# Kernel optimization log

Hardware: AMD Instinct MI355X
Metric: run time of the kernel (lower is better)

Reference implementation:

```python
import jax, jax.numpy as jnp
import numpy as np

# Fixed tetrahedral (kanchor=4) rotation->anchor permutation table, taken verbatim
# from the docstring in the original source (trace_idx_ori).
TRACE_IDX_ORI = jnp.array([
    [0, 1, 2, 3], [0, 2, 3, 1], [0, 3, 1, 2],
    [1, 2, 0, 3], [1, 0, 3, 2], [1, 3, 2, 0],
    [2, 3, 0, 1], [2, 0, 1, 3], [2, 1, 3, 0],
    [3, 1, 0, 2], [3, 0, 2, 1], [3, 2, 1, 0]], dtype=jnp.int32)

B, A, N, M, D, H = 1, 4, 384, 384, 256, 8
C = D // H  # d_model_per_head = 32
NR = TRACE_IDX_ORI.shape[0]  # 12 rotations


def _project_heads(x, W, b):
    # x: (b, a, n, d) -> (b, a, h, n, c)
    y = x @ W.T + b
    bb, aa, nn, _ = y.shape
    return y.reshape(bb, aa, nn, H, C).transpose(0, 1, 3, 2, 4)


def setup_inputs() -> dict:
    key = jax.random.key(0)
    ks = jax.random.split(key, 6)
    s = 1.0 / np.sqrt(D).astype(np.float32)
    return {
        "input_q": jax.random.normal(ks[0], (B, A, N, D), dtype=jnp.float32),
        "input_k": jax.random.normal(ks[1], (B, A, M, D), dtype=jnp.float32),
        "input_v": jax.random.normal(ks[2], (B, A, M, D), dtype=jnp.float32),
        "Wq": jax.random.normal(ks[3], (D, D), dtype=jnp.float32) * s,
        "bq": jnp.zeros((D,), dtype=jnp.float32),
        "Wk": jax.random.normal(ks[4], (D, D), dtype=jnp.float32) * s,
        "bk": jnp.zeros((D,), dtype=jnp.float32),
        "Wv": jax.random.normal(ks[5], (D, D), dtype=jnp.float32) * s,
        "bv": jnp.zeros((D,), dtype=jnp.float32),
    }


def reference(input_q, input_k, input_v, Wq, bq, Wk, bk, Wv, bv):
    # Step 0: linear projections + split heads.  q,k,v: (b, a, h, n|m, c)
    q = _project_heads(input_q, Wq, bq)
    k = _project_heads(input_k, Wk, bk)
    v = _project_heads(input_v, Wv, bv)

    # Step 1: per-anchor-pair local attention scores: (b, a, e, h, n, m)
    scores_ae = jnp.einsum('bahnc,behmc->baehnm', q, k) / jnp.sqrt(
        jnp.asarray(C, dtype=q.dtype))

    # Step 2: rotation-wise gather (attn_mode='r_soft', alternative_impl=False).
    # For rotation r, query anchor a attends to key anchor trace_idx_ori[r, a]:
    # scores_rot[b, r, a] = scores_ae[b, a, trace_idx_ori[r, a]]  -> (b, nr, a, h, n, m)
    a_idx = jnp.arange(A, dtype=jnp.int32)[None, :]  # (1, A) broadcasts vs (NR, A)
    scores_rot = scores_ae[:, a_idx, TRACE_IDX_ORI]

    # Global rotation attention: pool over anchors/heads/points (attn_r_summ='mean',
    # attn_r_multihead=False), make non-negative ('sq'), normalize over rotations.
    pooled = jnp.mean(scores_rot, axis=(2, 3, 4, 5))  # (b, nr)
    pos = pooled * pooled
    attn_r = pos / jnp.sum(pos, axis=-1, keepdims=True)  # (b, nr)

    # Step 3+4: softmax over key points per rotation, gather values per rotation,
    # then weight by the global rotation attention.
    attn_local = jax.nn.softmax(scores_rot, axis=-1)  # (b, nr, a, h, n, m)
    v_rot = v[:, TRACE_IDX_ORI]  # (b, nr, a, h, m, c)
    hidden = jnp.einsum('br,brahnm,brahmc->bahnc', attn_r, attn_local, v_rot)

    # Merge heads: (b, a, h, n, c) -> (b, a, n, h*c)
    out = hidden.transpose(0, 1, 3, 2, 4).reshape(B, A, N, D)
    return out
```

## Files before the change

kernel.cpp:

```cpp
#include <hip/hip_runtime.h>
#include <hip/hip_bf16.h>

typedef __attribute__((ext_vector_type(8))) short s8x8;
typedef __attribute__((ext_vector_type(4))) float f32x4;

__device__ __forceinline__ ushort f2bf(float x) {
    union { float f; unsigned u; } c; c.f = x;
    unsigned r = c.u + 0x7FFFu + ((c.u >> 16) & 1u);
    return (ushort)(r >> 16);
}
__device__ __forceinline__ float bf2f(ushort b) {
    union { unsigned u; float f; } c; c.u = ((unsigned)b) << 16;
    return c.f;
}

__global__ __launch_bounds__(128) void proj_mfma_kernel(
    const float* __restrict__ Xq, const float* __restrict__ Xk,
    const float* __restrict__ Xv,
    const float* __restrict__ Wq, const float* __restrict__ bq,
    const float* __restrict__ Wk, const float* __restrict__ bk,
    const float* __restrict__ Wv, const float* __restrict__ bv,
    ushort* __restrict__ qh, ushort* __restrict__ ql,
    ushort* __restrict__ kh, ushort* __restrict__ kl,
    ushort* __restrict__ vh)
{
    __shared__ ushort smem[2][16384];

    const int z = blockIdx.z;
    const float* X    = (z == 0) ? Xq : (z == 1) ? Xk : Xv;
    const float* W    = (z == 0) ? Wq : (z == 1) ? Wk : Wv;
    const float* bias = (z == 0) ? bq : (z == 1) ? bk : bv;

    const int tid  = threadIdx.x;
    const int row0 = blockIdx.x * 64;
    const int col0 = blockIdx.y * 64;

    #pragma unroll
    for (int i = 0; i < 32; ++i) {
        const int idx4 = tid + 128 * i;
        const int col  = idx4 >> 6;
        const int k4   = (idx4 & 63) * 4;
        const float4 wv = *(const float4*)&W[(col0 + col) * 256 + k4];
        const int kk = k4 >> 5;
        const int lg = (k4 >> 3) & 3;
        const int i0 = k4 & 7;
        const int base = ((kk * 4 + lg) * 64 + col) * 8 + i0;
        ushort hb[4], lb[4];
        const float w0[4] = {wv.x, wv.y, wv.z, wv.w};
        #pragma unroll
        for (int j = 0; j < 4; ++j) {
            hb[j] = f2bf(w0[j]);
            lb[j] = f2bf(w0[j] - bf2f(hb[j]));
        }
        *(uint2*)&smem[0][base] = *(const uint2*)&hb[0];
        *(uint2*)&smem[1][base] = *(const uint2*)&lb[0];
    }
    __syncthreads();

    const int wave = tid >> 6;
    const int lane = tid & 63;
    const int lg   = lane >> 4;
    const int ll   = lane & 15;

    f32x4 acc[2][4];
    #pragma unroll
    for (int r = 0; r < 2; ++r)
        #pragma unroll
        for (int c = 0; c < 4; ++c) acc[r][c] = (f32x4){0.f, 0.f, 0.f, 0.f};

    for (int kk = 0; kk < 8; ++kk) {
        s8x8 ah[2], al[2];
        #pragma unroll
        for (int rt = 0; rt < 2; ++rt) {
            const int row = row0 + wave * 32 + rt * 16 + ll;
            const float* xp = &X[(size_t)row * 256 + kk * 32 + lg * 8];
            const float4 x0 = *(const float4*)&xp[0];
            const float4 x1 = *(const float4*)&xp[4];
            const float xv[8] = {x0.x, x0.y, x0.z, x0.w, x1.x, x1.y, x1.z, x1.w};
            #pragma unroll
            for (int j = 0; j < 8; ++j) {
                const ushort hb = f2bf(xv[j]);
                ah[rt][j] = (short)hb;
                al[rt][j] = (short)f2bf(xv[j] - bf2f(hb));
            }
        }
        #pragma unroll
        for (int ct = 0; ct < 4; ++ct) {
            const int boff = ((kk * 4 + lg) * 64 + ct * 16 + ll) * 8;
            const s8x8 bh = *(const s8x8*)&smem[0][boff];
            const s8x8 bl = *(const s8x8*)&smem[1][boff];
            #pragma unroll
            for (int rt = 0; rt < 2; ++rt) {
                acc[rt][ct] = __builtin_amdgcn_mfma_f32_16x16x32_bf16(ah[rt], bh, acc[rt][ct], 0, 0, 0);
                acc[rt][ct] = __builtin_amdgcn_mfma_f32_16x16x32_bf16(al[rt], bh, acc[rt][ct], 0, 0, 0);
                acc[rt][ct] = __builtin_amdgcn_mfma_f32_16x16x32_bf16(ah[rt], bl, acc[rt][ct], 0, 0, 0);
            }
        }
    }

    float bct[4];
    #pragma unroll
    for (int ct = 0; ct < 4; ++ct) bct[ct] = bias[col0 + ct * 16 + ll];

    if (z != 2) {
        #pragma unroll
        for (int rt = 0; rt < 2; ++rt) {
            #pragma unroll
            for (int j = 0; j < 4; ++j) {
                const int row = row0 + wave * 32 + rt * 16 + lg * 4 + j;
                const int ae = row / 384;
                const int n = row - ae * 384;
                #pragma unroll
                for (int ct = 0; ct < 4; ++ct) {
                    const int d = col0 + ct * 16 + ll;
                    const int hd = d >> 5;
                    const int c = d & 31;
                    const float v = acc[rt][ct][j] + bct[ct];
                    const ushort hb = f2bf(v);
                    const ushort lb = f2bf(v - bf2f(hb));
                    if (z == 0) {
                        const size_t idx = ((size_t)((ae * 8 + hd) * 384 + n)) * 32 + c;
                        qh[idx] = hb; ql[idx] = lb;
                    } else {
                        const size_t idx =
                            ((size_t)(((ae * 8 + hd) * 4 + (c >> 3)) * 384 + n)) * 8 + (c & 7);
                        kh[idx] = hb; kl[idx] = lb;
                    }
                }
            }
        }
    } else {
        __syncthreads();
        float* T = (float*)&smem[0][0];
        #pragma unroll
        for (int rt = 0; rt < 2; ++rt)
            #pragma unroll
            for (int j = 0; j < 4; ++j) {
                const int rl = wave * 32 + rt * 16 + lg * 4 + j;
                #pragma unroll
                for (int ct = 0; ct < 4; ++ct)
                    T[rl * 65 + ct * 16 + ll] = acc[rt][ct][j] + bct[ct];
            }
        __syncthreads();
        const int col_l = tid >> 1;
        const int mh    = (tid & 1) * 32;
        const int d = col0 + col_l;
        const int hd = d >> 5;
        const int c = d & 31;
        const int e = row0 / 384;
        const int m0 = row0 - e * 384;
        ushort hbuf[32] __attribute__((aligned(16)));
        #pragma unroll
        for (int k32 = 0; k32 < 32; ++k32)
            hbuf[k32] = f2bf(T[(mh + k32) * 65 + col_l]);
        const size_t base = (size_t)((e * 8 + hd) * 32 + c) * 384 + m0 + mh;
        #pragma unroll
        for (int u = 0; u < 4; ++u)
            *(uint4*)&vh[base + u * 8] = *(const uint4*)&hbuf[u * 8];
    }
}

__global__ __launch_bounds__(192) void attn_mfma_kernel(
    const ushort* __restrict__ qhb, const ushort* __restrict__ qlb,
    const ushort* __restrict__ khb, const ushort* __restrict__ klb,
    const ushort* __restrict__ vhb,
    float* __restrict__ Sout, float* __restrict__ msum_part)
{
    __shared__ ushort Kh[4 * 192 * 8];
    __shared__ ushort Kl[4 * 192 * 8];
    __shared__ ushort Vh[32 * 200];
    __shared__ float  Pl[3][2][16][36];
    __shared__ float  red[192];

    const int strip = blockIdx.x;
    const int aeh   = blockIdx.y;
    const int hh    = aeh & 7;
    const int ee    = (aeh >> 3) & 3;
    const int aa    = aeh >> 5;
    const int e8h   = ee * 8 + hh;
    const int a8h   = aa * 8 + hh;
    const int tid   = threadIdx.x;
    const int wave  = tid >> 6;
    const int lane  = tid & 63;
    const int lg    = lane >> 4;
    const int ll    = lane & 15;

    s8x8 qfh[2], qfl[2];
    #pragma unroll
    for (int r = 0; r < 2; ++r) {
        const int n0 = strip * 96 + (2 * wave + r) * 16;
        const size_t off = (size_t)(a8h * 384 + n0 + ll) * 32 + lg * 8;
        qfh[r] = *(const s8x8*)&qhb[off];
        qfl[r] = *(const s8x8*)&qlb[off];
    }

    f32x4 oacc[2][2];
    #pragma unroll
    for (int r = 0; r < 2; ++r)
        #pragma unroll
        for (int ct = 0; ct < 2; ++ct)
            oacc[r][ct] = (f32x4){0.f, 0.f, 0.f, 0.f};
    float lsum[2][4];
    #pragma unroll
    for (int r = 0; r < 2; ++r)
        #pragma unroll
        for (int j = 0; j < 4; ++j) lsum[r][j] = 0.f;
    float rs = 0.f;
    const float sc = 0.17677669529663687f;

    for (int half = 0; half < 2; ++half) {
        #pragma unroll
        for (int i = 0; i < 4; ++i) {
            const size_t src = ((size_t)(e8h * 4 + i) * 384 + half * 192 + tid) * 8;
            *(uint4*)&Kh[(i * 192 + tid) * 8] = *(const uint4*)&khb[src];
            *(uint4*)&Kl[(i * 192 + tid) * 8] = *(const uint4*)&klb[src];
        }
        #pragma unroll
        for (int i = 0; i < 4; ++i) {
            const int u = tid + 192 * i;
            const int c = u / 24;
            const int m8 = (u - c * 24) * 8;
            *(uint4*)&Vh[c * 200 + m8] =
                *(const uint4*)&vhb[(size_t)(e8h * 32 + c) * 384 + half * 192 + m8];
        }
        __syncthreads();

        for (int mt2 = 0; mt2 < 6; ++mt2) {
            #pragma unroll
            for (int sub = 0; sub < 2; ++sub) {
                const int mt = mt2 * 2 + sub;
                const s8x8 kfh = *(const s8x8*)&Kh[(lg * 192 + mt * 16 + ll) * 8];
                const s8x8 kfl = *(const s8x8*)&Kl[(lg * 192 + mt * 16 + ll) * 8];
                #pragma unroll
                for (int r = 0; r < 2; ++r) {
                    f32x4 s = {0.f, 0.f, 0.f, 0.f};
                    __builtin_amdgcn_s_setprio(1);
                    s = __builtin_amdgcn_mfma_f32_16x16x32_bf16(qfh[r], kfh, s, 0, 0, 0);
                    s = __builtin_amdgcn_mfma_f32_16x16x32_bf16(qfl[r], kfh, s, 0, 0, 0);
                    s = __builtin_amdgcn_mfma_f32_16x16x32_bf16(qfh[r], kfl, s, 0, 0, 0);
                    __builtin_amdgcn_s_setprio(0);
                    rs += s[0] + s[1] + s[2] + s[3];
                    #pragma unroll
                    for (int j = 0; j < 4; ++j) {
                        const float p = __expf(s[j] * sc);
                        lsum[r][j] += p;
                        Pl[wave][r][lg * 4 + j][sub * 16 + ll] = p;
                    }
                }
            }
            const int mloc = mt2 * 32;
            const s8x8 vf0 = *(const s8x8*)&Vh[(0  + ll) * 200 + mloc + lg * 8];
            const s8x8 vf1 = *(const s8x8*)&Vh[(16 + ll) * 200 + mloc + lg * 8];
            #pragma unroll
            for (int r = 0; r < 2; ++r) {
                const float* prow = &Pl[wave][r][ll][lg * 8];
                s8x8 pah, pal;
                #pragma unroll
                for (int e2 = 0; e2 < 8; ++e2) {
                    const float pv = prow[e2];
                    const ushort hb = f2bf(pv);
                    pah[e2] = (short)hb;
                    pal[e2] = (short)f2bf(pv - bf2f(hb));
                }
                __builtin_amdgcn_s_setprio(1);
                oacc[r][0] = __builtin_amdgcn_mfma_f32_16x16x32_bf16(pah, vf0, oacc[r][0], 0, 0, 0);
                oacc[r][0] = __builtin_amdgcn_mfma_f32_16x16x32_bf16(pal, vf0, oacc[r][0], 0, 0, 0);
                oacc[r][1] = __builtin_amdgcn_mfma_f32_16x16x32_bf16(pah, vf1, oacc[r][1], 0, 0, 0);
                oacc[r][1] = __builtin_amdgcn_mfma_f32_16x16x32_bf16(pal, vf1, oacc[r][1], 0, 0, 0);
                __builtin_amdgcn_s_setprio(0);
            }
        }
        __syncthreads();
    }

    #pragma unroll
    for (int r = 0; r < 2; ++r) {
        #pragma unroll
        for (int j = 0; j < 4; ++j) {
            float L = lsum[r][j];
            L += __shfl_xor(L, 1);
            L += __shfl_xor(L, 2);
            L += __shfl_xor(L, 4);
            L += __shfl_xor(L, 8);
            const float invL = 1.f / L;
            const int row = strip * 96 + (2 * wave + r) * 16 + lg * 4 + j;
            const size_t base = (size_t)(aeh * 384 + row) * 32;
            Sout[base + 0  + ll] = oacc[r][0][j] * invL;
            Sout[base + 16 + ll] = oacc[r][1][j] * invL;
        }
    }

    red[tid] = rs * sc;
    __syncthreads();
    for (int off = 96; off >= 3; off >>= 1) {
        if (tid < off) red[tid] += red[tid + off];
        __syncthreads();
    }
    if (tid == 0) msum_part[aeh * 4 + strip] = red[0] + red[1] + red[2];
}

__global__ __launch_bounds__(256) void stats_kernel(
    const float* __restrict__ msum_part, float* __restrict__ wout)
{
    __shared__ float sh[128];
    __shared__ float cell[16];
    const int tid = threadIdx.x;
    if (tid < 128) {
        float s = 0.f;
        #pragma unroll
        for (int j = 0; j < 4; ++j) s += msum_part[tid * 4 + j];
        sh[tid] = s;
    }
    __syncthreads();
    if (tid < 16) {
        const int base = (tid >> 2) * 32 + (tid & 3) * 8;
        float s = 0.f;
        #pragma unroll
        for (int hh = 0; hh < 8; ++hh) s += sh[base + hh];
        cell[tid] = s;
    }
    __syncthreads();
    if (tid == 0) {
        const int TR[12][4] = {
            {0,1,2,3},{0,2,3,1},{0,3,1,2},{1,2,0,3},{1,0,3,2},{1,3,2,0},
            {2,3,0,1},{2,0,1,3},{2,1,3,0},{3,1,0,2},{3,0,2,1},{3,2,1,0}};
        const float denom = 4.0f * 8.0f * 384.0f * 384.0f;
        float pos[12];
        float psum = 0.f;
        for (int r = 0; r < 12; ++r) {
            float s = 0.f;
            for (int aa = 0; aa < 4; ++aa) s += cell[aa * 4 + TR[r][aa]];
            const float pooled = s / denom;
            pos[r] = pooled * pooled;
            psum += pos[r];
        }
        float w[16];
        for (int i = 0; i < 16; ++i) w[i] = 0.f;
        const float ip = 1.f / psum;
        for (int r = 0; r < 12; ++r)
            for (int aa = 0; aa < 4; ++aa) w[aa * 4 + TR[r][aa]] += pos[r] * ip;
        for (int i = 0; i < 16; ++i) wout[i] = w[i];
    }
}

__global__ __launch_bounds__(256) void combine_kernel(
    const float* __restrict__ S, const float* __restrict__ w,
    float* __restrict__ out)
{
    const int idx = blockIdx.x * 256 + threadIdx.x;
    const int a = idx / 98304;
    const int rem = idx - a * 98304;
    const int n = rem >> 8;
    const int d = rem & 255;
    const int h = d >> 5;
    const int c = d & 31;
    float r = 0.f;
    #pragma unroll
    for (int e = 0; e < 4; ++e)
        r += w[a * 4 + e] * S[(size_t)(((a * 4 + e) * 8 + h) * 384 + n) * 32 + c];
    out[idx] = r;
}

extern "C" void kernel_launch(void* const* d_in, const int* in_sizes, int n_in,
                              void* d_out, int out_size, void* d_ws, size_t ws_size,
                              hipStream_t stream)
{
    const float* in_q = (const float*)d_in[0];
    const float* in_k = (const float*)d_in[1];
    const float* in_v = (const float*)d_in[2];
    const float* Wq   = (const float*)d_in[3];
    const float* bq   = (const float*)d_in[4];
    const float* Wk   = (const float*)d_in[5];
    const float* bk   = (const float*)d_in[6];
    const float* Wv   = (const float*)d_in[7];
    const float* bv   = (const float*)d_in[8];

    const size_t NE = 393216;
    ushort* qh = (ushort*)d_ws;
    ushort* ql = qh + NE;
    ushort* kh = ql + NE;
    ushort* kl = kh + NE;
    ushort* vh = kl + NE;
    float*  Sb = (float*)((char*)d_ws + 5 * NE * sizeof(ushort));
    float*  ms = Sb + 1572864;
    float*  wb = ms + 512;
    float*  outp = (float*)d_out;

    dim3 pgrid(24, 4, 3);
    proj_mfma_kernel<<<pgrid, 128, 0, stream>>>(in_q, in_k, in_v, Wq, bq, Wk, bk,
                                                Wv, bv, qh, ql, kh, kl, vh);
    dim3 agrid(4, 128);
    attn_mfma_kernel<<<agrid, 192, 0, stream>>>(qh, ql, kh, kl, vh, Sb, ms);
    stats_kernel<<<1, 256, 0, stream>>>(ms, wb);
    combine_kernel<<<1536, 256, 0, stream>>>(Sb, wb, outp);
}
```

Baseline: 43.39 us.

## Compute rotation pooling from projection column sums, drop stats kernel and P split

The projection kernel now reads W directly from global memory instead of staging it in LDS, uses packed bf16 conversions, writes V with vector stores, and emits per-column partial sums of q and k. Because the mean of q·k over n and m factors into (sum q)·(sum k), the per-score reduction in attention and the separate stats kernel are removed, and the rotation weights are computed inside a vectorized combine kernel. In attention, P is stored as a single bf16 value rather than a hi/lo pair, which halves the PV MFMAs but lowers softmax-weight precision. The K LDS layout also gets padding to reduce bank conflicts.

```diff
diff --git a/kernel.cpp b/kernel.cpp
--- a/kernel.cpp
+++ b/kernel.cpp
@@ -3,6 +3,8 @@
 
 typedef __attribute__((ext_vector_type(8))) short s8x8;
 typedef __attribute__((ext_vector_type(4))) float f32x4;
+
+union FragU { s8x8 v; unsigned d[4]; };
 
 __device__ __forceinline__ ushort f2bf(float x) {
     union { float f; unsigned u; } c; c.f = x;
@@ -13,8 +15,16 @@
     union { unsigned u; float f; } c; c.u = ((unsigned)b) << 16;
     return c.f;
 }
-
-__global__ __launch_bounds__(128) void proj_mfma_kernel(
+__device__ __forceinline__ unsigned cvt_pk(float lo, float hi) {
+    unsigned r;
+    asm("v_cvt_pk_bf16_f32 %0, %1, %2" : "=v"(r) : "v"(lo), "v"(hi));
+    return r;
+}
+__device__ __forceinline__ float asf(unsigned u) {
+    union { unsigned u; float f; } c; c.u = u; return c.f;
+}
+
+__global__ __launch_bounds__(256) void proj_kernel(
     const float* __restrict__ Xq, const float* __restrict__ Xk,
     const float* __restrict__ Xv,
     const float* __restrict__ Wq, const float* __restrict__ bq,
@@ -22,9 +32,9 @@
     const float* __restrict__ Wv, const float* __restrict__ bv,
     ushort* __restrict__ qh, ushort* __restrict__ ql,
     ushort* __restrict__ kh, ushort* __restrict__ kl,
-    ushort* __restrict__ vh)
+    ushort* __restrict__ vh, float* __restrict__ part)
 {
-    __shared__ ushort smem[2][16384];
+    __shared__ float csum[4][64];
 
     const int z = blockIdx.z;
     const float* X    = (z == 0) ? Xq : (z == 1) ? Xk : Xv;
@@ -32,72 +42,60 @@
     const float* bias = (z == 0) ? bq : (z == 1) ? bk : bv;
 
     const int tid  = threadIdx.x;
-    const int row0 = blockIdx.x * 64;
-    const int col0 = blockIdx.y * 64;
-
-    #pragma unroll
-    for (int i = 0; i < 32; ++i) {
-        const int idx4 = tid + 128 * i;
-        const int col  = idx4 >> 6;
-        const int k4   = (idx4 & 63) * 4;
-        const float4 wv = *(const float4*)&W[(col0 + col) * 256 + k4];
-        const int kk = k4 >> 5;
-        const int lg = (k4 >> 3) & 3;
-        const int i0 = k4 & 7;
-        const int base = ((kk * 4 + lg) * 64 + col) * 8 + i0;
-        ushort hb[4], lb[4];
-        const float w0[4] = {wv.x, wv.y, wv.z, wv.w};
-        #pragma unroll
-        for (int j = 0; j < 4; ++j) {
-            hb[j] = f2bf(w0[j]);
-            lb[j] = f2bf(w0[j] - bf2f(hb[j]));
-        }
-        *(uint2*)&smem[0][base] = *(const uint2*)&hb[0];
-        *(uint2*)&smem[1][base] = *(const uint2*)&lb[0];
-    }
-    __syncthreads();
-
     const int wave = tid >> 6;
     const int lane = tid & 63;
     const int lg   = lane >> 4;
     const int ll   = lane & 15;
+    const int row0 = blockIdx.x * 128 + wave * 32;
+    const int col0 = blockIdx.y * 64;
 
     f32x4 acc[2][4];
     #pragma unroll
-    for (int r = 0; r < 2; ++r)
-        #pragma unroll
-        for (int c = 0; c < 4; ++c) acc[r][c] = (f32x4){0.f, 0.f, 0.f, 0.f};
+    for (int rt = 0; rt < 2; ++rt)
+        #pragma unroll
+        for (int ct = 0; ct < 4; ++ct) acc[rt][ct] = (f32x4){0.f, 0.f, 0.f, 0.f};
 
     for (int kk = 0; kk < 8; ++kk) {
-        s8x8 ah[2], al[2];
+        FragU ah[2], al[2];
         #pragma unroll
         for (int rt = 0; rt < 2; ++rt) {
-            const int row = row0 + wave * 32 + rt * 16 + ll;
-            const float* xp = &X[(size_t)row * 256 + kk * 32 + lg * 8];
+            const float* xp = &X[(size_t)(row0 + rt * 16 + ll) * 256 + kk * 32 + lg * 8];
             const float4 x0 = *(const float4*)&xp[0];
             const float4 x1 = *(const float4*)&xp[4];
             const float xv[8] = {x0.x, x0.y, x0.z, x0.w, x1.x, x1.y, x1.z, x1.w};
             #pragma unroll
-            for (int j = 0; j < 8; ++j) {
-                const ushort hb = f2bf(xv[j]);
-                ah[rt][j] = (short)hb;
-                al[rt][j] = (short)f2bf(xv[j] - bf2f(hb));
+            for (int i = 0; i < 4; ++i) {
+                const unsigned hd = cvt_pk(xv[2 * i], xv[2 * i + 1]);
+                ah[rt].d[i] = hd;
+                al[rt].d[i] = cvt_pk(xv[2 * i]     - asf(hd << 16),
+                                     xv[2 * i + 1] - asf(hd & 0xffff0000u));
             }
         }
         #pragma unroll
         for (int ct = 0; ct < 4; ++ct) {
-            const int boff = ((kk * 4 + lg) * 64 + ct * 16 + ll) * 8;
-            const s8x8 bh = *(const s8x8*)&smem[0][boff];
-            const s8x8 bl = *(const s8x8*)&smem[1][boff];
+            const float* wp = &W[(size_t)(col0 + ct * 16 + ll) * 256 + kk * 32 + lg * 8];
+            const float4 w0 = *(const float4*)&wp[0];
+            const float4 w1 = *(const float4*)&wp[4];
+            const float wv[8] = {w0.x, w0.y, w0.z, w0.w, w1.x, w1.y, w1.z, w1.w};
+            FragU bh, bl;
+            #pragma unroll
+            for (int i = 0; i < 4; ++i) {
+                const unsigned hd = cvt_pk(wv[2 * i], wv[2 * i + 1]);
+                bh.d[i] = hd;
+                bl.d[i] = cvt_pk(wv[2 * i]     - asf(hd << 16),
+                                 wv[2 * i + 1] - asf(hd & 0xffff0000u));
+            }
             #pragma unroll
             for (int rt = 0; rt < 2; ++rt) {
-                acc[rt][ct] = __builtin_amdgcn_mfma_f32_16x16x32_bf16(ah[rt], bh, acc[rt][ct], 0, 0, 0);
-                acc[rt][ct] = __builtin_amdgcn_mfma_f32_16x16x32_bf16(al[rt], bh, acc[rt][ct], 0, 0, 0);
-                acc[rt][ct] = __builtin_amdgcn_mfma_f32_16x16x32_bf16(ah[rt], bl, acc[rt][ct], 0, 0, 0);
-            }
-        }
-    }
-
+                acc[rt][ct] = __builtin_amdgcn_mfma_f32_16x16x32_bf16(ah[rt].v, bh.v, acc[rt][ct], 0, 0, 0);
+                acc[rt][ct] = __builtin_amdgcn_mfma_f32_16x16x32_bf16(al[rt].v, bh.v, acc[rt][ct], 0, 0, 0);
+                acc[rt][ct] = __builtin_amdgcn_mfma_f32_16x16x32_bf16(ah[rt].v, bl.v, acc[rt][ct], 0, 0, 0);
+            }
+        }
+    }
+
+    const int bx = blockIdx.x;
+    const int ae = bx / 3;
     float bct[4];
     #pragma unroll
     for (int ct = 0; ct < 4; ++ct) bct[ct] = bias[col0 + ct * 16 + ll];
@@ -106,15 +104,13 @@
         #pragma unroll
         for (int rt = 0; rt < 2; ++rt) {
             #pragma unroll
-            for (int j = 0; j < 4; ++j) {
-                const int row = row0 + wave * 32 + rt * 16 + lg * 4 + j;
-                const int ae = row / 384;
-                const int n = row - ae * 384;
+            for (int ct = 0; ct < 4; ++ct) {
+                const int d = col0 + ct * 16 + ll;
+                const int hd = d >> 5;
+                const int c = d & 31;
                 #pragma unroll
-                for (int ct = 0; ct < 4; ++ct) {
-                    const int d = col0 + ct * 16 + ll;
-                    const int hd = d >> 5;
-                    const int c = d & 31;
+                for (int j = 0; j < 4; ++j) {
+                    const int n = (bx - ae * 3) * 128 + wave * 32 + rt * 16 + lg * 4 + j;
                     const float v = acc[rt][ct][j] + bct[ct];
                     const ushort hb = f2bf(v);
                     const ushort lb = f2bf(v - bf2f(hb));
@@ -129,48 +125,52 @@
                 }
             }
         }
+        #pragma unroll
+        for (int ct = 0; ct < 4; ++ct) {
+            float cs = 8.f * bct[ct];
+            #pragma unroll
+            for (int rt = 0; rt < 2; ++rt)
+                #pragma unroll
+                for (int j = 0; j < 4; ++j) cs += acc[rt][ct][j];
+            cs += __shfl_xor(cs, 16);
+            cs += __shfl_xor(cs, 32);
+            if (lg == 0) csum[wave][ct * 16 + ll] = cs;
+        }
+        __syncthreads();
+        if (tid < 64) {
+            const float s = csum[0][tid] + csum[1][tid] + csum[2][tid] + csum[3][tid];
+            part[((size_t)(z * 4 + ae) * 3 + (bx - ae * 3)) * 256 + blockIdx.y * 64 + tid] = s;
+        }
     } else {
-        __syncthreads();
-        float* T = (float*)&smem[0][0];
-        #pragma unroll
-        for (int rt = 0; rt < 2; ++rt)
-            #pragma unroll
-            for (int j = 0; j < 4; ++j) {
-                const int rl = wave * 32 + rt * 16 + lg * 4 + j;
+        #pragma unroll
+        for (int rt = 0; rt < 2; ++rt) {
+            #pragma unroll
+            for (int ct = 0; ct < 4; ++ct) {
+                const int d = col0 + ct * 16 + ll;
+                const int hd = d >> 5;
+                const int c = d & 31;
+                ushort p[4];
                 #pragma unroll
-                for (int ct = 0; ct < 4; ++ct)
-                    T[rl * 65 + ct * 16 + ll] = acc[rt][ct][j] + bct[ct];
-            }
-        __syncthreads();
-        const int col_l = tid >> 1;
-        const int mh    = (tid & 1) * 32;
-        const int d = col0 + col_l;
-        const int hd = d >> 5;
-        const int c = d & 31;
-        const int e = row0 / 384;
-        const int m0 = row0 - e * 384;
-        ushort hbuf[32] __attribute__((aligned(16)));
-        #pragma unroll
-        for (int k32 = 0; k32 < 32; ++k32)
-            hbuf[k32] = f2bf(T[(mh + k32) * 65 + col_l]);
-        const size_t base = (size_t)((e * 8 + hd) * 32 + c) * 384 + m0 + mh;
-        #pragma unroll
-        for (int u = 0; u < 4; ++u)
-            *(uint4*)&vh[base + u * 8] = *(const uint4*)&hbuf[u * 8];
+                for (int j = 0; j < 4; ++j) p[j] = f2bf(acc[rt][ct][j] + bct[ct]);
+                const int m0 = (bx - ae * 3) * 128 + wave * 32 + rt * 16 + lg * 4;
+                const size_t basei = ((size_t)((ae * 8 + hd) * 32 + c)) * 384 + m0;
+                *(uint2*)&vh[basei] =
+                    make_uint2((unsigned)p[0] | ((unsigned)p[1] << 16),
+                               (unsigned)p[2] | ((unsigned)p[3] << 16));
+            }
+        }
     }
 }
 
 __global__ __launch_bounds__(192) void attn_mfma_kernel(
     const ushort* __restrict__ qhb, const ushort* __restrict__ qlb,
     const ushort* __restrict__ khb, const ushort* __restrict__ klb,
-    const ushort* __restrict__ vhb,
-    float* __restrict__ Sout, float* __restrict__ msum_part)
+    const ushort* __restrict__ vhb, float* __restrict__ Sout)
 {
-    __shared__ ushort Kh[4 * 192 * 8];
-    __shared__ ushort Kl[4 * 192 * 8];
+    __shared__ ushort Kh[4 * 1544];
+    __shared__ ushort Kl[4 * 1544];
     __shared__ ushort Vh[32 * 200];
-    __shared__ float  Pl[3][2][16][36];
-    __shared__ float  red[192];
+    __shared__ ushort Pl[3 * 2 * 16 * 40];
 
     const int strip = blockIdx.x;
     const int aeh   = blockIdx.y;
@@ -205,15 +205,14 @@
     for (int r = 0; r < 2; ++r)
         #pragma unroll
         for (int j = 0; j < 4; ++j) lsum[r][j] = 0.f;
-    float rs = 0.f;
     const float sc = 0.17677669529663687f;
 
     for (int half = 0; half < 2; ++half) {
         #pragma unroll
         for (int i = 0; i < 4; ++i) {
             const size_t src = ((size_t)(e8h * 4 + i) * 384 + half * 192 + tid) * 8;
-            *(uint4*)&Kh[(i * 192 + tid) * 8] = *(const uint4*)&khb[src];
-            *(uint4*)&Kl[(i * 192 + tid) * 8] = *(const uint4*)&klb[src];
+            *(uint4*)&Kh[i * 1544 + tid * 8] = *(const uint4*)&khb[src];
+            *(uint4*)&Kl[i * 1544 + tid * 8] = *(const uint4*)&klb[src];
         }
         #pragma unroll
         for (int i = 0; i < 4; ++i) {
@@ -229,8 +228,8 @@
             #pragma unroll
             for (int sub = 0; sub < 2; ++sub) {
                 const int mt = mt2 * 2 + sub;
-                const s8x8 kfh = *(const s8x8*)&Kh[(lg * 192 + mt * 16 + ll) * 8];
-                const s8x8 kfl = *(const s8x8*)&Kl[(lg * 192 + mt * 16 + ll) * 8];
+                const s8x8 kfh = *(const s8x8*)&Kh[lg * 1544 + (mt * 16 + ll) * 8];
+                const s8x8 kfl = *(const s8x8*)&Kl[lg * 1544 + (mt * 16 + ll) * 8];
                 #pragma unroll
                 for (int r = 0; r < 2; ++r) {
                     f32x4 s = {0.f, 0.f, 0.f, 0.f};
@@ -239,12 +238,11 @@
                     s = __builtin_amdgcn_mfma_f32_16x16x32_bf16(qfl[r], kfh, s, 0, 0, 0);
                     s = __builtin_amdgcn_mfma_f32_16x16x32_bf16(qfh[r], kfl, s, 0, 0, 0);
                     __builtin_amdgcn_s_setprio(0);
-                    rs += s[0] + s[1] + s[2] + s[3];
                     #pragma unroll
                     for (int j = 0; j < 4; ++j) {
                         const float p = __expf(s[j] * sc);
                         lsum[r][j] += p;
-                        Pl[wave][r][lg * 4 + j][sub * 16 + ll] = p;
+                        Pl[((wave * 2 + r) * 16 + lg * 4 + j) * 40 + sub * 16 + ll] = f2bf(p);
                     }
                 }
             }
@@ -253,20 +251,10 @@
             const s8x8 vf1 = *(const s8x8*)&Vh[(16 + ll) * 200 + mloc + lg * 8];
             #pragma unroll
             for (int r = 0; r < 2; ++r) {
-                const float* prow = &Pl[wave][r][ll][lg * 8];
-                s8x8 pah, pal;
-                #pragma unroll
-                for (int e2 = 0; e2 < 8; ++e2) {
-                    const float pv = prow[e2];
-                    const ushort hb = f2bf(pv);
-                    pah[e2] = (short)hb;
-                    pal[e2] = (short)f2bf(pv - bf2f(hb));
-                }
+                const s8x8 pa = *(const s8x8*)&Pl[((wave * 2 + r) * 16 + ll) * 40 + lg * 8];
                 __builtin_amdgcn_s_setprio(1);
-                oacc[r][0] = __builtin_amdgcn_mfma_f32_16x16x32_bf16(pah, vf0, oacc[r][0], 0, 0, 0);
-                oacc[r][0] = __builtin_amdgcn_mfma_f32_16x16x32_bf16(pal, vf0, oacc[r][0], 0, 0, 0);
-                oacc[r][1] = __builtin_amdgcn_mfma_f32_16x16x32_bf16(pah, vf1, oacc[r][1], 0, 0, 0);
-                oacc[r][1] = __builtin_amdgcn_mfma_f32_16x16x32_bf16(pal, vf1, oacc[r][1], 0, 0, 0);
+                oacc[r][0] = __builtin_amdgcn_mfma_f32_16x16x32_bf16(pa, vf0, oacc[r][0], 0, 0, 0);
+                oacc[r][1] = __builtin_amdgcn_mfma_f32_16x16x32_bf16(pa, vf1, oacc[r][1], 0, 0, 0);
                 __builtin_amdgcn_s_setprio(0);
             }
         }
@@ -289,36 +277,42 @@
             Sout[base + 16 + ll] = oacc[r][1][j] * invL;
         }
     }
-
-    red[tid] = rs * sc;
+}
+
+__global__ __launch_bounds__(256) void combine_kernel(
+    const float* __restrict__ S, const float* __restrict__ part,
+    float* __restrict__ out)
+{
+    __shared__ float ws4[4][16];
+    __shared__ float cellsh[16];
+    __shared__ float wsh[16];
+    const int tid = threadIdx.x;
+    const int lane = tid & 63;
+    const int wv = tid >> 6;
+
+    float qs[4], ks[4];
+    #pragma unroll
+    for (int a2 = 0; a2 < 4; ++a2) {
+        const float* pq = &part[(size_t)(0 * 4 + a2) * 3 * 256 + tid];
+        const float* pk = &part[(size_t)(1 * 4 + a2) * 3 * 256 + tid];
+        qs[a2] = pq[0] + pq[256] + pq[512];
+        ks[a2] = pk[0] + pk[256] + pk[512];
+    }
+    #pragma unroll
+    for (int i = 0; i < 16; ++i) {
+        float v = qs[i >> 2] * ks[i & 3];
+        v += __shfl_xor(v, 1);
+        v += __shfl_xor(v, 2);
+        v += __shfl_xor(v, 4);
+        v += __shfl_xor(v, 8);
+        v += __shfl_xor(v, 16);
+        v += __shfl_xor(v, 32);
+        if (lane == 0) ws4[wv][i] = v;
+    }
     __syncthreads();
-    for (int off = 96; off >= 3; off >>= 1) {
-        if (tid < off) red[tid] += red[tid + off];
-        __syncthreads();
-    }
-    if (tid == 0) msum_part[aeh * 4 + strip] = red[0] + red[1] + red[2];
-}
-
-__global__ __launch_bounds__(256) void stats_kernel(
-    const float* __restrict__ msum_part, float* __restrict__ wout)
-{
-    __shared__ float sh[128];
-    __shared__ float cell[16];
-    const int tid = threadIdx.x;
-    if (tid < 128) {
-        float s = 0.f;
-        #pragma unroll
-        for (int j = 0; j < 4; ++j) s += msum_part[tid * 4 + j];
-        sh[tid] = s;
-    }
-    __syncthreads();
-    if (tid < 16) {
-        const int base = (tid >> 2) * 32 + (tid & 3) * 8;
-        float s = 0.f;
-        #pragma unroll
-        for (int hh = 0; hh < 8; ++hh) s += sh[base + hh];
-        cell[tid] = s;
-    }
+    if (tid < 16)
+        cellsh[tid] = 0.17677669529663687f *
+            (ws4[0][tid] + ws4[1][tid] + ws4[2][tid] + ws4[3][tid]);
     __syncthreads();
     if (tid == 0) {
         const int TR[12][4] = {
@@ -329,7 +323,7 @@
         float psum = 0.f;
         for (int r = 0; r < 12; ++r) {
             float s = 0.f;
-            for (int aa = 0; aa < 4; ++aa) s += cell[aa * 4 + TR[r][aa]];
+            for (int a2 = 0; a2 < 4; ++a2) s += cellsh[a2 * 4 + TR[r][a2]];
             const float pooled = s / denom;
             pos[r] = pooled * pooled;
             psum += pos[r];
@@ -338,27 +332,26 @@
         for (int i = 0; i < 16; ++i) w[i] = 0.f;
         const float ip = 1.f / psum;
         for (int r = 0; r < 12; ++r)
-            for (int aa = 0; aa < 4; ++aa) w[aa * 4 + TR[r][aa]] += pos[r] * ip;
-        for (int i = 0; i < 16; ++i) wout[i] = w[i];
-    }
-}
-
-__global__ __launch_bounds__(256) void combine_kernel(
-    const float* __restrict__ S, const float* __restrict__ w,
-    float* __restrict__ out)
-{
-    const int idx = blockIdx.x * 256 + threadIdx.x;
-    const int a = idx / 98304;
-    const int rem = idx - a * 98304;
-    const int n = rem >> 8;
-    const int d = rem & 255;
-    const int h = d >> 5;
-    const int c = d & 31;
-    float r = 0.f;
-    #pragma unroll
-    for (int e = 0; e < 4; ++e)
-        r += w[a * 4 + e] * S[(size_t)(((a * 4 + e) * 8 + h) * 384 + n) * 32 + c];
-    out[idx] = r;
+            for (int a2 = 0; a2 < 4; ++a2) w[a2 * 4 + TR[r][a2]] += pos[r] * ip;
+        for (int i = 0; i < 16; ++i) wsh[i] = w[i];
+    }
+    __syncthreads();
+
+    const int idx4 = blockIdx.x * 256 + tid;
+    const int a = idx4 / 24576;
+    const int rem = idx4 - a * 24576;
+    const int n = rem >> 6;
+    const int d4 = rem & 63;
+    const int h = d4 >> 3;
+    const int c0 = (d4 & 7) * 4;
+    float4 r = make_float4(0.f, 0.f, 0.f, 0.f);
+    #pragma unroll
+    for (int e = 0; e < 4; ++e) {
+        const float wv2 = wsh[a * 4 + e];
+        const float4 s = *(const float4*)&S[(size_t)(((a * 4 + e) * 8 + h) * 384 + n) * 32 + c0];
+        r.x += wv2 * s.x; r.y += wv2 * s.y; r.z += wv2 * s.z; r.w += wv2 * s.w;
+    }
+    *(float4*)&out[(size_t)idx4 * 4] = r;
 }
 
 extern "C" void kernel_launch(void* const* d_in, const int* in_sizes, int n_in,
@@ -375,22 +368,19 @@
     const float* Wv   = (const float*)d_in[7];
     const float* bv   = (const float*)d_in[8];
 
-    const size_t NE = 393216;
     ushort* qh = (ushort*)d_ws;
-    ushort* ql = qh + NE;
-    ushort* kh = ql + NE;
-    ushort* kl = kh + NE;
-    ushort* vh = kl + NE;
-    float*  Sb = (float*)((char*)d_ws + 5 * NE * sizeof(ushort));
-    float*  ms = Sb + 1572864;
-    float*  wb = ms + 512;
+    ushort* ql = qh + 393216;
+    ushort* kh = ql + 393216;
+    ushort* kl = kh + 393216;
+    ushort* vh = kl + 393216;
+    float*  Sb = (float*)(vh + 393216);
+    float*  pt = Sb + 1572864;
     float*  outp = (float*)d_out;
 
-    dim3 pgrid(24, 4, 3);
-    proj_mfma_kernel<<<pgrid, 128, 0, stream>>>(in_q, in_k, in_v, Wq, bq, Wk, bk,
-                                                Wv, bv, qh, ql, kh, kl, vh);
+    dim3 pgrid(12, 4, 3);
+    proj_kernel<<<pgrid, 256, 0, stream>>>(in_q, in_k, in_v, Wq, bq, Wk, bk,
+                                           Wv, bv, qh, ql, kh, kl, vh, pt);
     dim3 agrid(4, 128);
-    attn_mfma_kernel<<<agrid, 192, 0, stream>>>(qh, ql, kh, kl, vh, Sb, ms);
-    stats_kernel<<<1, 256, 0, stream>>>(ms, wb);
-    combine_kernel<<<1536, 256, 0, stream>>>(Sb, wb, outp);
-}
+    attn_mfma_kernel<<<agrid, 192, 0, stream>>>(qh, ql, kh, kl, vh, Sb);
+    combine_kernel<<<384, 256, 0, stream>>>(Sb, pt, outp);
+}
```

Result: slower. 47.23 us (+8.9%).
